# Performance work log

Measured on AMD Instinct MI355X. Metric: run time of the kernel, lower is better.

The kernel has to match this reference:

```python
import jax, jax.numpy as jnp
import numpy as np
from jax import lax

# Shapes / module constants
B, N = 16, 1048576          # batch, events per sample (multiple of S)
H, W = 256, 256             # sensor resolution (init dim)
S = 32                      # temporal segments (hardcoded in forward)
START = 2                   # self.startIdx
SEG = N // S                # events per segment


def setup_inputs() -> dict:
    key = jax.random.key(0)
    k1, k2 = jax.random.split(key)
    xs = jax.random.randint(k1, (B, N), 0, W, dtype=jnp.int32)
    ys = jax.random.randint(k2, (B, N), 0, H, dtype=jnp.int32)
    # self.blurFilterKernel: center 0.5, surround 0.0625 (shared across groups)
    blur_kernel = jnp.array(
        [0.0625, 0.0625, 0.0625, 0.0625, 0.5, 0.0625, 0.0625, 0.0625, 0.0625],
        dtype=jnp.float32).reshape(3, 3)
    return {"xs": xs, "ys": ys, "blur_kernel": blur_kernel}


def _aligned_shift(coord, dimlen, blur_kernel):
    """Per-segment histogram along one spatial axis -> clamp -> blur -> centroid
    alignment. coord: [B, N] int32 in [0, dimlen). Returns [B, S] int32 shifts."""
    chunks = jnp.repeat(jnp.arange(S, dtype=jnp.int32), SEG)      # [N]
    idx = coord + dimlen * chunks[None, :]                         # [B, N]
    hist = jax.vmap(
        lambda i: jnp.zeros(S * dimlen, jnp.int32).at[i].add(1))(idx)
    hist = hist.astype(jnp.float32)                                # [B, S*dimlen]
    mean = hist.mean(axis=-1, keepdims=True)
    std = jnp.std(hist, axis=-1, ddof=1, keepdims=True)            # torch unbiased std
    hist = jnp.clip(hist, 0.0, mean + 3.0 * std)
    img = hist.reshape(B, 1, S, dimlen)
    # grouped conv with identical kernel per group == single-channel conv
    blurred = lax.conv_general_dilated(
        img, blur_kernel.reshape(1, 1, 3, 3), (1, 1), ((1, 1), (1, 1)))
    blurred = blurred.reshape(B, S, dimlen)
    m = jnp.einsum('bsw,w->bs', blurred,
                   jnp.arange(dimlen, dtype=jnp.float32)) / float(SEG)
    start = m[:, START:START + 1]
    # aligned = m - start - (dimlen//2 - start)
    aligned = jnp.round(m - start - (dimlen // 2 - start)).astype(jnp.int32)
    return aligned


def _accumulate(idx_c, idx_v):
    """Adaptive accumulation for one batch element.
    idx_c: [S, SEG] container indices, idx_v: [S, SEG] verifier indices."""
    container = jnp.zeros(W * H, jnp.int32).at[idx_c[START]].add(1)
    verifier = jnp.zeros((W // 2) * (H // 2), bool).at[idx_v[START]].set(True)

    def step(carry, seg):
        cont, ver, active = carry
        ic, iv = seg
        v_new = ver.at[iv].set(True)
        new_cnt = v_new.sum().astype(jnp.float32)
        xor_cnt = jnp.logical_xor(v_new, ver).sum().astype(jnp.float32)
        # original breaks when new_info ratio < 0.01 (segment NOT added)
        proceed = active & (xor_cnt / new_cnt >= 0.01)
        cont = jnp.where(proceed, cont.at[ic].add(1), cont)
        ver = jnp.where(proceed, v_new, ver)
        return (cont, ver, proceed), None

    (container, _, _), _ = lax.scan(
        step, (container, verifier, jnp.bool_(True)),
        (idx_c[START + 1:], idx_v[START + 1:]))
    return container


def _forward(xs, ys, blur_kernel):
    alignedX = _aligned_shift(xs, W, blur_kernel)   # [B, S]
    alignedY = _aligned_shift(ys, H, blur_kernel)   # [B, S]
    shX = jnp.repeat(alignedX, SEG, axis=1)          # [B, N]
    shY = jnp.repeat(alignedY, SEG, axis=1)
    xsft = jnp.clip(xs - shX, 0, W - 1)
    ysft = jnp.clip(ys - shY, 0, H - 1)
    idx_c = (xsft + W * ysft).reshape(B, S, SEG)
    idx_v = (xsft // 2 + (W // 2) * (ysft // 2)).reshape(B, S, SEG)
    containers = jax.vmap(_accumulate)(idx_c, idx_v)  # [B, W*H]
    return containers.reshape(B, 1, H, W).astype(jnp.float32)


def reference(xs, ys, blur_kernel):
    return _forward(xs, ys, blur_kernel)
```

## Files before the change

kernel.cpp:

```cpp
#include <hip/hip_runtime.h>
#include <cstdint>
#include <cstddef>

#define BB 16
#define NTOT 1048576
#define SS 32
#define SEG 32768
#define DIM 256
#define VW 512

#define OFF_HX   0u
#define OFF_HY   524288u
#define OFF_BM0  1048576u
#define OFF_AX   2097152u
#define OFF_AY   2099200u
#define OFF_PR   2101248u
#define OFF_STG  2138112u

__device__ __forceinline__ int clamp255(int v) {
    return v < 0 ? 0 : (v > 255 ? 255 : v);
}

__global__ __launch_bounds__(256) void k_hist4(const int* __restrict__ xs,
                                               const int* __restrict__ ys,
                                               uint32_t* __restrict__ histX,
                                               uint32_t* __restrict__ histY,
                                               uint32_t* __restrict__ staging) {
    int blk = blockIdx.x;
    int arr = blk & 1;
    int s = (blk >> 1) & 31;
    int b = blk >> 6;
    int t = threadIdx.x;
    staging[(size_t)blk * 512 + t] = 0u;
    staging[(size_t)blk * 512 + 256 + t] = 0u;

    const int* src = arr ? ys : xs;
    uint32_t* dst = arr ? histY : histX;
    __shared__ uint32_t ph[256][32];
    uint32_t* phl = (uint32_t*)ph;
#pragma unroll
    for (int i = 0; i < 32; ++i) phl[t + i * 256] = 0u;
    __syncthreads();
    int c = t & 31;
    const int4* p4 = (const int4*)(src + (size_t)b * NTOT + (size_t)s * SEG);
#pragma unroll 8
    for (int i = 0; i < 32; ++i) {
        int4 v = p4[i * 256 + t];
        atomicAdd(&ph[v.x][c], 1u);
        atomicAdd(&ph[v.y][c], 1u);
        atomicAdd(&ph[v.z][c], 1u);
        atomicAdd(&ph[v.w][c], 1u);
    }
    __syncthreads();
    uint32_t sum = 0u;
#pragma unroll
    for (int j = 0; j < 32; ++j)
        sum += ph[t][(j + t) & 31];
    dst[(size_t)(b * SS + s) * 256 + t] = sum;
}

__global__ __launch_bounds__(512) void k_shifts(const uint32_t* __restrict__ histX,
                                                const uint32_t* __restrict__ histY,
                                                const float* __restrict__ blurk,
                                                int* __restrict__ alignedX,
                                                int* __restrict__ alignedY) {
    int blk = blockIdx.x;
    int b = blk >> 1, axis = blk & 1;
    const uint32_t* hist = (axis == 0 ? histX : histY) + (size_t)b * SS * DIM;
    int* out = (axis == 0 ? alignedX : alignedY) + b * SS;

    __shared__ float vals[SS][DIM];
    __shared__ double wsq[8];
    __shared__ float mrow[SS];
    int t = threadIdx.x;
    int w = t >> 6, lane = t & 63;
    int c0 = lane << 2;

    double lsq = 0.0;
    for (int r = w; r < SS; r += 8) {
        uint4 u = *(const uint4*)(hist + r * DIM + c0);
        float v0 = (float)u.x, v1 = (float)u.y, v2 = (float)u.z, v3 = (float)u.w;
        vals[r][c0 + 0] = v0; vals[r][c0 + 1] = v1;
        vals[r][c0 + 2] = v2; vals[r][c0 + 3] = v3;
        double d0 = (double)v0 - 128.0, d1 = (double)v1 - 128.0;
        double d2 = (double)v2 - 128.0, d3 = (double)v3 - 128.0;
        lsq += d0 * d0 + d1 * d1 + d2 * d2 + d3 * d3;
    }
    for (int o = 32; o > 0; o >>= 1) lsq += __shfl_xor(lsq, o, 64);
    if (lane == 0) wsq[w] = lsq;
    __syncthreads();
    float s2 = (float)(wsq[0] + wsq[1] + wsq[2] + wsq[3]
                     + wsq[4] + wsq[5] + wsq[6] + wsq[7]);
    float sd = sqrtf(s2 / 8191.0f);
    float thr = 128.0f + 3.0f * sd;

    float k00 = blurk[0], k01 = blurk[1], k02 = blurk[2];
    float k10 = blurk[3], k11 = blurk[4], k12 = blurk[5];
    float k20 = blurk[6], k21 = blurk[7], k22 = blurk[8];

#define V(r, c) fminf(vals[r][c], thr)
    for (int s = w; s < SS; s += 8) {
        double dot = 0.0;
#pragma unroll
        for (int j = 0; j < 4; ++j) {
            int c = c0 + j;
            int cm = c - 1, cp = c + 1;
            bool cml = (cm >= 0), cpl = (cp < DIM);
            float bsum = 0.0f;
            if (s - 1 >= 0) {
                if (cml) bsum += k00 * V(s - 1, cm);
                bsum += k01 * V(s - 1, c);
                if (cpl) bsum += k02 * V(s - 1, cp);
            }
            if (cml) bsum += k10 * V(s, cm);
            bsum += k11 * V(s, c);
            if (cpl) bsum += k12 * V(s, cp);
            if (s + 1 < SS) {
                if (cml) bsum += k20 * V(s + 1, cm);
                bsum += k21 * V(s + 1, c);
                if (cpl) bsum += k22 * V(s + 1, cp);
            }
            dot += (double)bsum * (double)c;
        }
        for (int o = 32; o > 0; o >>= 1) dot += __shfl_xor(dot, o, 64);
        if (lane == 0) mrow[s] = (float)(dot / 32768.0);
    }
#undef V
    __syncthreads();

    if (t < SS) {
        float start = mrow[2];
        float a = mrow[t] - start;
        float c = 128.0f - start;
        out[t] = (int)rintf(a - c);
    }
}

__global__ __launch_bounds__(256) void k_bitmap_g(const int* __restrict__ xs,
                                                  const int* __restrict__ ys,
                                                  const int* __restrict__ aX,
                                                  const int* __restrict__ aY,
                                                  uint32_t* __restrict__ bmp) {
    int blk = blockIdx.x;
    int p = blk & 1;
    int sl = (blk >> 1) & 7;
    int b = blk >> 4;
    int s = 2 + sl;
    int shx = aX[b * SS + s];
    int shy = aY[b * SS + s];
    __shared__ uint32_t bm[VW];
    int t = threadIdx.x;
    bm[t] = 0u; bm[t + 256] = 0u;
    __syncthreads();
    size_t base = (size_t)b * NTOT + (size_t)s * SEG + (size_t)p * (SEG / 2);
    const int4* x4 = (const int4*)(xs + base);
    const int4* y4 = (const int4*)(ys + base);
    for (int i = 0; i < 16; ++i) {
        int4 xv = x4[i * 256 + t];
        int4 yv = y4[i * 256 + t];
#define DOV(xc, yc) { int xf = clamp255((xc) - shx); int yf = clamp255((yc) - shy); \
                      int iv = (xf >> 1) + ((yf >> 1) << 7); \
                      atomicOr(&bm[iv >> 5], 1u << (iv & 31)); }
        DOV(xv.x, yv.x) DOV(xv.y, yv.y) DOV(xv.z, yv.z) DOV(xv.w, yv.w)
#undef DOV
    }
    __syncthreads();
    uint32_t* outp = bmp + ((size_t)(b * 8 + sl) * 2 + p) * VW;
    outp[t] = bm[t];
    outp[t + 256] = bm[t + 256];
}

__global__ __launch_bounds__(256) void k_scan_tail(const int* __restrict__ xs,
                                                   const int* __restrict__ ys,
                                                   const int* __restrict__ aX,
                                                   const int* __restrict__ aY,
                                                   const uint32_t* __restrict__ bmp,
                                                   int* __restrict__ proceed) {
    int b = blockIdx.x;
    int t = threadIdx.x;
    __shared__ uint32_t ver[VW];
    __shared__ uint32_t bm[VW];
    __shared__ int wred[4];
    __shared__ int sh_flag;
    __shared__ int sh_total;

    for (int i = t; i < 30; i += 256) proceed[b * SS + 2 + i] = 0;
    int active = 1;
    const uint32_t* base = bmp + (size_t)b * 8 * 2 * VW;
    int wid = t >> 6, lane = t & 63;

    {
        uint32_t w0 = base[t] | base[VW + t];
        uint32_t w1 = base[t + 256] | base[VW + t + 256];
        ver[t] = w0; ver[t + 256] = w1;
        int c = __popc(w0) + __popc(w1);
        for (int o = 32; o > 0; o >>= 1) c += __shfl_down(c, o, 64);
        if (lane == 0) wred[wid] = c;
        __syncthreads();
        if (t == 0) {
            sh_total = wred[0] + wred[1] + wred[2] + wred[3];
            proceed[b * SS + 2] = 1;
        }
    }
    __syncthreads();

    for (int sl = 1; sl < 8; ++sl) {
        uint32_t w0 = base[(size_t)(sl * 2) * VW + t]
                    | base[(size_t)(sl * 2 + 1) * VW + t];
        uint32_t w1 = base[(size_t)(sl * 2) * VW + t + 256]
                    | base[(size_t)(sl * 2 + 1) * VW + t + 256];
        int c = __popc(w0 & ~ver[t]) + __popc(w1 & ~ver[t + 256]);
        for (int o = 32; o > 0; o >>= 1) c += __shfl_down(c, o, 64);
        if (lane == 0) wred[wid] = c;
        __syncthreads();
        if (t == 0) {
            int newly = wred[0] + wred[1] + wred[2] + wred[3];
            int total = sh_total + newly;
            float ratio = (float)newly / (float)total;
            int f = (ratio >= 0.01f) ? 1 : 0;
            sh_flag = f;
            if (f) {
                sh_total = total;
                proceed[b * SS + 2 + sl] = 1;
            }
        }
        __syncthreads();
        if (!sh_flag) { active = 0; break; }
        ver[t] |= w0;
        ver[t + 256] |= w1;
        __syncthreads();
    }
    if (!active) return;

    for (int s = 10; s < SS; ++s) {
        int shx = aX[b * SS + s];
        int shy = aY[b * SS + s];
        bm[t] = 0u; bm[t + 256] = 0u;
        __syncthreads();
        const int4* x4 = (const int4*)(xs + (size_t)b * NTOT + (size_t)s * SEG);
        const int4* y4 = (const int4*)(ys + (size_t)b * NTOT + (size_t)s * SEG);
        for (int i = 0; i < 32; ++i) {
            int4 xv = x4[i * 256 + t];
            int4 yv = y4[i * 256 + t];
#define DOV(xc, yc) { int xf = clamp255((xc) - shx); int yf = clamp255((yc) - shy); \
                      int iv = (xf >> 1) + ((yf >> 1) << 7); \
                      atomicOr(&bm[iv >> 5], 1u << (iv & 31)); }
            DOV(xv.x, yv.x) DOV(xv.y, yv.y) DOV(xv.z, yv.z) DOV(xv.w, yv.w)
#undef DOV
        }
        __syncthreads();
        uint32_t w0 = bm[t], w1 = bm[t + 256];
        int c = __popc(w0 & ~ver[t]) + __popc(w1 & ~ver[t + 256]);
        for (int o = 32; o > 0; o >>= 1) c += __shfl_down(c, o, 64);
        if (lane == 0) wred[wid] = c;
        __syncthreads();
        if (t == 0) {
            int newly = wred[0] + wred[1] + wred[2] + wred[3];
            int total = sh_total + newly;
            float ratio = (float)newly / (float)total;
            int f = (ratio >= 0.01f) ? 1 : 0;
            sh_flag = f;
            if (f) {
                sh_total = total;
                proceed[b * SS + s] = 1;
            }
        }
        __syncthreads();
        if (!sh_flag) break;
        ver[t] |= w0;
        ver[t + 256] |= w1;
        __syncthreads();
    }
}

__global__ __launch_bounds__(1024) void k_accum7(const int* __restrict__ xs,
                                                 const int* __restrict__ ys,
                                                 const int* __restrict__ aX,
                                                 const int* __restrict__ aY,
                                                 const int* __restrict__ proceed,
                                                 uint32_t* __restrict__ staging) {
    int blk = blockIdx.x;
    int p = blk & 7, half = (blk >> 3) & 1, b = blk >> 4;
    __shared__ uint32_t acc[16384];
    int t = threadIdx.x;
    for (int i = t; i < 16384; i += 1024) acc[i] = 0u;
    __syncthreads();
    int ybase = half << 7;
    for (int s = 2; s < SS; ++s) {
        if (!proceed[b * SS + s]) continue;
        int shx = aX[b * SS + s];
        int shy = aY[b * SS + s];
        size_t base = (size_t)b * NTOT + (size_t)s * SEG + (size_t)p * 4096;
        int4 xv = ((const int4*)(xs + base))[t];
        int4 yv = ((const int4*)(ys + base))[t];
#define DOC(xc, yc) { int xf = clamp255((xc) - shx); int yf = clamp255((yc) - shy); \
                      if ((yf >> 7) == half) { \
                          int cell = xf + ((yf - ybase) << 8); \
                          atomicAdd(&acc[cell >> 1], 1u << ((cell & 1) << 4)); } }
        DOC(xv.x, yv.x) DOC(xv.y, yv.y) DOC(xv.z, yv.z) DOC(xv.w, yv.w)
#undef DOC
    }
    __syncthreads();
    uint32_t* stg = staging + (size_t)b * 32768 + ((size_t)half << 14);
    for (int i = t; i < 16384; i += 1024) {
        uint32_t w = acc[i];
        if (w) atomicAdd(&stg[i], w);
    }
}

__global__ __launch_bounds__(1024) void k_convert(const uint32_t* __restrict__ staging,
                                                  float* __restrict__ out) {
    int g = blockIdx.x * 1024 + threadIdx.x;
    uint32_t w = staging[g];
    ((float2*)out)[g] = make_float2((float)(w & 0xFFFFu), (float)(w >> 16));
}

extern "C" void kernel_launch(void* const* d_in, const int* in_sizes, int n_in,
                              void* d_out, int out_size, void* d_ws, size_t ws_size,
                              hipStream_t stream) {
    const int* xs = (const int*)d_in[0];
    const int* ys = (const int*)d_in[1];
    const float* blurk = (const float*)d_in[2];
    float* out = (float*)d_out;

    uint8_t* ws = (uint8_t*)d_ws;
    uint32_t* histX = (uint32_t*)(ws + OFF_HX);
    uint32_t* histY = (uint32_t*)(ws + OFF_HY);
    int* aX = (int*)(ws + OFF_AX);
    int* aY = (int*)(ws + OFF_AY);
    int* proceed = (int*)(ws + OFF_PR);
    uint32_t* bm0 = (uint32_t*)(ws + OFF_BM0);
    uint32_t* staging = (uint32_t*)(ws + OFF_STG);

    k_hist4<<<BB * SS * 2, 256, 0, stream>>>(xs, ys, histX, histY, staging);
    k_shifts<<<BB * 2, 512, 0, stream>>>(histX, histY, blurk, aX, aY);
    k_bitmap_g<<<BB * 8 * 2, 256, 0, stream>>>(xs, ys, aX, aY, bm0);
    k_scan_tail<<<BB, 256, 0, stream>>>(xs, ys, aX, aY, bm0, proceed);
    k_accum7<<<BB * 2 * 8, 1024, 0, stream>>>(xs, ys, aX, aY, proceed, staging);
    k_convert<<<512, 1024, 0, stream>>>(staging, out);
}
```

Measured before the change: 66.11 us.

## Split histogram into four partial blocks per segment and move staging zeroing

The histogram kernel now launches four times as many blocks, each covering a quarter of a segment and writing partial histograms. k_shifts sums the four partials on load. Zeroing of the staging buffer moves from the histogram kernel into the bitmap kernel, and the workspace layout is reorganised so that the bitmap and staging regions overlap the partial-histogram region. The aim is more parallelism and better occupancy in the first pass, at the cost of extra shared-memory init per block and more partial data to read.

```diff
diff --git a/kernel.cpp b/kernel.cpp
--- a/kernel.cpp
+++ b/kernel.cpp
@@ -9,42 +9,40 @@
 #define DIM 256
 #define VW 512
 
-#define OFF_HX   0u
-#define OFF_HY   524288u
-#define OFF_BM0  1048576u
-#define OFF_AX   2097152u
-#define OFF_AY   2099200u
-#define OFF_PR   2101248u
-#define OFF_STG  2138112u
+#define OFF_PHX  0u
+#define OFF_PHY  2097152u
+#define OFF_BM0  0u
+#define OFF_STG  1048576u
+#define OFF_AX   4194304u
+#define OFF_AY   4196352u
+#define OFF_PR   4198400u
 
 __device__ __forceinline__ int clamp255(int v) {
     return v < 0 ? 0 : (v > 255 ? 255 : v);
 }
 
-__global__ __launch_bounds__(256) void k_hist4(const int* __restrict__ xs,
+__global__ __launch_bounds__(256) void k_hist6(const int* __restrict__ xs,
                                                const int* __restrict__ ys,
-                                               uint32_t* __restrict__ histX,
-                                               uint32_t* __restrict__ histY,
-                                               uint32_t* __restrict__ staging) {
+                                               uint32_t* __restrict__ phX,
+                                               uint32_t* __restrict__ phY) {
     int blk = blockIdx.x;
-    int arr = blk & 1;
-    int s = (blk >> 1) & 31;
-    int b = blk >> 6;
-    int t = threadIdx.x;
-    staging[(size_t)blk * 512 + t] = 0u;
-    staging[(size_t)blk * 512 + 256 + t] = 0u;
-
+    int p = blk & 3;
+    int arr = (blk >> 2) & 1;
+    int s = (blk >> 3) & 31;
+    int b = blk >> 8;
+    int t = threadIdx.x;
     const int* src = arr ? ys : xs;
-    uint32_t* dst = arr ? histY : histX;
+    uint32_t* dst = arr ? phY : phX;
     __shared__ uint32_t ph[256][32];
     uint32_t* phl = (uint32_t*)ph;
 #pragma unroll
     for (int i = 0; i < 32; ++i) phl[t + i * 256] = 0u;
     __syncthreads();
     int c = t & 31;
-    const int4* p4 = (const int4*)(src + (size_t)b * NTOT + (size_t)s * SEG);
-#pragma unroll 8
-    for (int i = 0; i < 32; ++i) {
+    const int4* p4 = (const int4*)(src + (size_t)b * NTOT + (size_t)s * SEG
+                                   + (size_t)p * 8192);
+#pragma unroll
+    for (int i = 0; i < 8; ++i) {
         int4 v = p4[i * 256 + t];
         atomicAdd(&ph[v.x][c], 1u);
         atomicAdd(&ph[v.y][c], 1u);
@@ -56,17 +54,17 @@
 #pragma unroll
     for (int j = 0; j < 32; ++j)
         sum += ph[t][(j + t) & 31];
-    dst[(size_t)(b * SS + s) * 256 + t] = sum;
-}
-
-__global__ __launch_bounds__(512) void k_shifts(const uint32_t* __restrict__ histX,
-                                                const uint32_t* __restrict__ histY,
+    dst[((size_t)(b * SS + s) * 4 + p) * 256 + t] = sum;
+}
+
+__global__ __launch_bounds__(512) void k_shifts(const uint32_t* __restrict__ phX,
+                                                const uint32_t* __restrict__ phY,
                                                 const float* __restrict__ blurk,
                                                 int* __restrict__ alignedX,
                                                 int* __restrict__ alignedY) {
     int blk = blockIdx.x;
     int b = blk >> 1, axis = blk & 1;
-    const uint32_t* hist = (axis == 0 ? histX : histY) + (size_t)b * SS * DIM;
+    const uint32_t* hist = (axis == 0 ? phX : phY) + (size_t)b * SS * 4 * 256;
     int* out = (axis == 0 ? alignedX : alignedY) + b * SS;
 
     __shared__ float vals[SS][DIM];
@@ -78,8 +76,16 @@
 
     double lsq = 0.0;
     for (int r = w; r < SS; r += 8) {
-        uint4 u = *(const uint4*)(hist + r * DIM + c0);
-        float v0 = (float)u.x, v1 = (float)u.y, v2 = (float)u.z, v3 = (float)u.w;
+        const uint32_t* hr = hist + (size_t)(r * 4) * 256 + c0;
+        uint4 a0 = *(const uint4*)(hr);
+        uint4 a1 = *(const uint4*)(hr + 256);
+        uint4 a2 = *(const uint4*)(hr + 512);
+        uint4 a3 = *(const uint4*)(hr + 768);
+        uint32_t u0 = a0.x + a1.x + a2.x + a3.x;
+        uint32_t u1 = a0.y + a1.y + a2.y + a3.y;
+        uint32_t u2 = a0.z + a1.z + a2.z + a3.z;
+        uint32_t u3 = a0.w + a1.w + a2.w + a3.w;
+        float v0 = (float)u0, v1 = (float)u1, v2 = (float)u2, v3 = (float)u3;
         vals[r][c0 + 0] = v0; vals[r][c0 + 1] = v1;
         vals[r][c0 + 2] = v2; vals[r][c0 + 3] = v3;
         double d0 = (double)v0 - 128.0, d1 = (double)v1 - 128.0;
@@ -140,16 +146,22 @@
                                                   const int* __restrict__ ys,
                                                   const int* __restrict__ aX,
                                                   const int* __restrict__ aY,
-                                                  uint32_t* __restrict__ bmp) {
+                                                  uint32_t* __restrict__ bmp,
+                                                  uint32_t* __restrict__ staging) {
     int blk = blockIdx.x;
     int p = blk & 1;
     int sl = (blk >> 1) & 7;
     int b = blk >> 4;
+    int t = threadIdx.x;
+    {
+        uint32_t* stg = staging + (size_t)blk * 2048;
+#pragma unroll
+        for (int i = 0; i < 8; ++i) stg[t + i * 256] = 0u;
+    }
     int s = 2 + sl;
     int shx = aX[b * SS + s];
     int shy = aY[b * SS + s];
     __shared__ uint32_t bm[VW];
-    int t = threadIdx.x;
     bm[t] = 0u; bm[t + 256] = 0u;
     __syncthreads();
     size_t base = (size_t)b * NTOT + (size_t)s * SEG + (size_t)p * (SEG / 2);
@@ -324,17 +336,17 @@
     float* out = (float*)d_out;
 
     uint8_t* ws = (uint8_t*)d_ws;
-    uint32_t* histX = (uint32_t*)(ws + OFF_HX);
-    uint32_t* histY = (uint32_t*)(ws + OFF_HY);
+    uint32_t* phX = (uint32_t*)(ws + OFF_PHX);
+    uint32_t* phY = (uint32_t*)(ws + OFF_PHY);
     int* aX = (int*)(ws + OFF_AX);
     int* aY = (int*)(ws + OFF_AY);
     int* proceed = (int*)(ws + OFF_PR);
     uint32_t* bm0 = (uint32_t*)(ws + OFF_BM0);
     uint32_t* staging = (uint32_t*)(ws + OFF_STG);
 
-    k_hist4<<<BB * SS * 2, 256, 0, stream>>>(xs, ys, histX, histY, staging);
-    k_shifts<<<BB * 2, 512, 0, stream>>>(histX, histY, blurk, aX, aY);
-    k_bitmap_g<<<BB * 8 * 2, 256, 0, stream>>>(xs, ys, aX, aY, bm0);
+    k_hist6<<<BB * SS * 2 * 4, 256, 0, stream>>>(xs, ys, phX, phY);
+    k_shifts<<<BB * 2, 512, 0, stream>>>(phX, phY, blurk, aX, aY);
+    k_bitmap_g<<<BB * 8 * 2, 256, 0, stream>>>(xs, ys, aX, aY, bm0, staging);
     k_scan_tail<<<BB, 256, 0, stream>>>(xs, ys, aX, aY, bm0, proceed);
     k_accum7<<<BB * 2 * 8, 1024, 0, stream>>>(xs, ys, aX, aY, proceed, staging);
     k_convert<<<512, 1024, 0, stream>>>(staging, out);
```

Measured after the change: 67.15 us. Within noise of the previous version (+1.6%).
